# Performance work log

Measured on AMD Instinct MI355X. Metric: run time of the kernel, lower is better.

The kernel has to match this reference:

```python
import math
import jax, jax.numpy as jnp
import numpy as np

B, H, HKV, L, S, D = 1, 32, 8, 2048, 2048, 128
N_REP = H // HKV          # 4
SCALE = 1.0 / math.sqrt(D)


def setup_inputs() -> dict:
    key = jax.random.key(0)
    k1, k2, k3, k4 = jax.random.split(key, 4)
    query = jax.random.normal(k1, (B, H, L, D), dtype=jnp.float32)
    k_ = jax.random.normal(k2, (B, HKV, S, D), dtype=jnp.float32)
    v_ = jax.random.normal(k3, (B, HKV, S, D), dtype=jnp.float32)
    attn_mask = jax.random.normal(k4, (B, 1, L, S), dtype=jnp.float32)
    return {"query": query, "key": k_, "value": v_, "attn_mask": attn_mask}


def reference(query, key, value, attn_mask):
    # repeat_kv: Q -> [B, HKV, n_rep, L, D]; K/V stay [B, HKV, S, D]
    # (the torch code reshapes K/V to [B, HKV, 1, S, D]; broadcasting via
    # einsum is equivalent), mask unsqueezed at dim 1 -> [B, 1, 1, L, S].
    q = query.reshape(B, HKV, N_REP, L, D)
    scores = jnp.einsum("bkrld,bksd->bkrls", q, key)          # [B,HKV,n_rep,L,S]
    scores = scores + attn_mask[:, None]                        # broadcast add
    # softmax_fp8(x, dim=-1, invAttnHead=1/sqrt(D)) scales input by invAttnHead
    w = jax.nn.softmax(scores * SCALE, axis=-1)
    # dropout_p = 0.0 -> identity
    out = jnp.einsum("bkrls,bksd->bkrld", w, value)             # [B,HKV,n_rep,L,D]
    return out
```

## Files before the change

### kernel.cpp

```cpp
#include <hip/hip_runtime.h>

#define NH   32
#define NKV  8
#define LQ   2048
#define SK   2048
#define DH   128
#define BM   128
#define BN   64
#define KSTRIDE 136
#define VSTRIDE 72

typedef __attribute__((ext_vector_type(8)))  short bf8;
typedef __attribute__((ext_vector_type(4)))  float f4;
typedef __attribute__((ext_vector_type(16))) float f16v;

#if __has_builtin(__builtin_amdgcn_exp2f)
#define EXP2F(x) __builtin_amdgcn_exp2f(x)
#else
#define EXP2F(x) exp2f(x)
#endif

__device__ __forceinline__ unsigned int f2bf(float f) {
    unsigned int u = __builtin_bit_cast(unsigned int, f);
    u = (u + 0x7FFFu + ((u >> 16) & 1u)) >> 16;
    return u;
}

__global__ __launch_bounds__(256) void convert_k_kernel(
    const float* __restrict__ K, unsigned short* __restrict__ Kb)
{
    size_t base = ((size_t)blockIdx.x * 256 + threadIdx.x) * 8;
    float4 a = *(const float4*)(K + base);
    float4 b = *(const float4*)(K + base + 4);
    bf8 o;
    o[0] = (short)f2bf(a.x); o[1] = (short)f2bf(a.y);
    o[2] = (short)f2bf(a.z); o[3] = (short)f2bf(a.w);
    o[4] = (short)f2bf(b.x); o[5] = (short)f2bf(b.y);
    o[6] = (short)f2bf(b.z); o[7] = (short)f2bf(b.w);
    *(bf8*)(Kb + base) = o;
}

__global__ __launch_bounds__(256) void transpose_v_kernel(
    const float* __restrict__ V, unsigned short* __restrict__ VTb)
{
    __shared__ __align__(16) unsigned short Vl[DH * VSTRIDE];
    const int tid = threadIdx.x;
    const int kv  = blockIdx.x >> 5;
    const int s0  = (blockIdx.x & 31) * 64;
    const float* Vh = V + (size_t)kv * SK * DH;

    #pragma unroll
    for (int i = 0; i < 8; ++i) {
        int idx = tid * 4 + i * 1024;
        int s = idx >> 7, d = idx & 127;
        const float4 v4 = *(const float4*)(Vh + (size_t)(s0 + s) * DH + d);
        Vl[(d + 0) * VSTRIDE + s] = (unsigned short)f2bf(v4.x);
        Vl[(d + 1) * VSTRIDE + s] = (unsigned short)f2bf(v4.y);
        Vl[(d + 2) * VSTRIDE + s] = (unsigned short)f2bf(v4.z);
        Vl[(d + 3) * VSTRIDE + s] = (unsigned short)f2bf(v4.w);
    }
    __syncthreads();
    unsigned short* out = VTb + (size_t)kv * DH * SK;
    #pragma unroll
    for (int i = 0; i < 4; ++i) {
        int c = tid + i * 256;
        int d = c >> 3, s8 = (c & 7) * 8;
        *(bf8*)(out + (size_t)d * SK + s0 + s8) = *(const bf8*)(Vl + d * VSTRIDE + s8);
    }
}

__global__ __launch_bounds__(256, 2) void fattn_kernel(
    const float* __restrict__ Q, const unsigned short* __restrict__ Kb,
    const unsigned short* __restrict__ VTb, const float* __restrict__ M,
    float* __restrict__ O)
{
    __shared__ __align__(16) unsigned short Klds[2][BN * KSTRIDE];
    __shared__ __align__(16) unsigned short Vlds[2][DH * VSTRIDE];

    const int tid  = threadIdx.x;
    const int wave = tid >> 6;
    const int lane = tid & 63;
    const int l32  = lane & 31;
    const int hh   = lane >> 5;

    const int bx = blockIdx.x;
    const int h  = bx >> 4;
    const int lt = bx & 15;
    const int q0 = lt * BM;
    const int kv = h >> 2;

    const float*          Qh  = Q   + (size_t)h  * LQ * DH;
    const unsigned short* Kh  = Kb  + (size_t)kv * SK * DH;
    const unsigned short* VTh = VTb + (size_t)kv * DH * SK;

    const int sK0 = tid >> 4,        dK0 = (tid & 15) * 8;
    const int dV0 = tid >> 3,        sV0 = (tid & 7) * 8;

    const int qrow = q0 + wave * 32 + l32;
    const float* Mq = M + (size_t)qrow * SK;

    bf8 bQ[8];
    #pragma unroll
    for (int ks = 0; ks < 8; ++ks) {
        const float* qp = Qh + (size_t)qrow * DH + ks * 16 + hh * 8;
        float4 a = *(const float4*)(qp);
        float4 b = *(const float4*)(qp + 4);
        bQ[ks][0] = (short)f2bf(a.x); bQ[ks][1] = (short)f2bf(a.y);
        bQ[ks][2] = (short)f2bf(a.z); bQ[ks][3] = (short)f2bf(a.w);
        bQ[ks][4] = (short)f2bf(b.x); bQ[ks][5] = (short)f2bf(b.y);
        bQ[ks][6] = (short)f2bf(b.z); bQ[ks][7] = (short)f2bf(b.w);
    }

    f16v accO[4];
    #pragma unroll
    for (int nt = 0; nt < 4; ++nt)
        #pragma unroll
        for (int r = 0; r < 16; ++r) accO[nt][r] = 0.f;
    float lpart = 0.f;

    const float scale_log2e = 0.08838834764831845f * 1.4426950408889634f;

    bf8 kf[4], vf[4];
    #pragma unroll
    for (int c = 0; c < 4; ++c) {
        kf[c] = *(const bf8*)(Kh + (size_t)(sK0 + c * 16) * DH + dK0);
        vf[c] = *(const bf8*)(VTh + (size_t)(dV0 + c * 32) * SK + sV0);
    }
    #pragma unroll
    for (int c = 0; c < 4; ++c) {
        *(bf8*)(&Klds[0][(sK0 + c * 16) * KSTRIDE + dK0]) = kf[c];
        *(bf8*)(&Vlds[0][(dV0 + c * 32) * VSTRIDE + sV0]) = vf[c];
    }
    #pragma unroll
    for (int c = 0; c < 4; ++c) {
        kf[c] = *(const bf8*)(Kh + (size_t)(BN + sK0 + c * 16) * DH + dK0);
        vf[c] = *(const bf8*)(VTh + (size_t)(dV0 + c * 32) * SK + BN + sV0);
    }

    int buf = 0;
    for (int s0i = 0; s0i < SK; s0i += BN, buf ^= 1) {
        __syncthreads();

        float4 mv[2][4];
        #pragma unroll
        for (int mt = 0; mt < 2; ++mt)
            #pragma unroll
            for (int grp = 0; grp < 4; ++grp)
                mv[mt][grp] = *(const float4*)(Mq + s0i + mt * 32 + grp * 8 + hh * 4);

        const unsigned short* Kc = Klds[buf];
        const unsigned short* Vc = Vlds[buf];
        f16v accS[2];
        #pragma unroll
        for (int mt = 0; mt < 2; ++mt) {
            f16v a;
            #pragma unroll
            for (int r = 0; r < 16; ++r) a[r] = 0.f;
            #pragma unroll
            for (int ks = 0; ks < 8; ++ks) {
                bf8 aK = *(const bf8*)(Kc + (mt * 32 + l32) * KSTRIDE + ks * 16 + hh * 8);
                a = __builtin_amdgcn_mfma_f32_32x32x16_bf16(aK, bQ[ks], a, 0, 0, 0);
            }
            accS[mt] = a;
        }

        if (s0i + BN < SK) {
            #pragma unroll
            for (int c = 0; c < 4; ++c) {
                *(bf8*)(&Klds[buf ^ 1][(sK0 + c * 16) * KSTRIDE + dK0]) = kf[c];
                *(bf8*)(&Vlds[buf ^ 1][(dV0 + c * 32) * VSTRIDE + sV0]) = vf[c];
            }
            if (s0i + 2 * BN < SK) {
                #pragma unroll
                for (int c = 0; c < 4; ++c) {
                    kf[c] = *(const bf8*)(Kh + (size_t)(s0i + 2 * BN + sK0 + c * 16) * DH + dK0);
                    vf[c] = *(const bf8*)(VTh + (size_t)(dV0 + c * 32) * SK + s0i + 2 * BN + sV0);
                }
            }
        }

        unsigned int W[2][4][2];
        #pragma unroll
        for (int mt = 0; mt < 2; ++mt) {
            #pragma unroll
            for (int g = 0; g < 4; ++g) {
                float e0 = EXP2F((accS[mt][g * 4 + 0] + mv[mt][g].x) * scale_log2e);
                float e1 = EXP2F((accS[mt][g * 4 + 1] + mv[mt][g].y) * scale_log2e);
                float e2 = EXP2F((accS[mt][g * 4 + 2] + mv[mt][g].z) * scale_log2e);
                float e3 = EXP2F((accS[mt][g * 4 + 3] + mv[mt][g].w) * scale_log2e);
                lpart += (e0 + e1) + (e2 + e3);
                W[mt][g][0] = f2bf(e0) | (f2bf(e1) << 16);
                W[mt][g][1] = f2bf(e2) | (f2bf(e3) << 16);
            }
        }
        unsigned int R[2][4][2];
        #pragma unroll
        for (int mt = 0; mt < 2; ++mt)
            #pragma unroll
            for (int g = 0; g < 4; ++g)
                #pragma unroll
                for (int b = 0; b < 2; ++b)
                    R[mt][g][b] = (unsigned int)__shfl_xor((int)W[mt][g][b], 32);

        bf8 bP[4];
        #pragma unroll
        for (int ks = 0; ks < 4; ++ks) {
            const int mt = ks >> 1, b = (ks & 1) * 2;
            unsigned int lo0 = hh ? R[mt][b + 1][0] : W[mt][b][0];
            unsigned int lo1 = hh ? R[mt][b + 1][1] : W[mt][b][1];
            unsigned int hi0 = hh ? W[mt][b + 1][0] : R[mt][b][0];
            unsigned int hi1 = hh ? W[mt][b + 1][1] : R[mt][b][1];
            uint4 u = {lo0, lo1, hi0, hi1};
            bP[ks] = __builtin_bit_cast(bf8, u);
        }

        #pragma unroll
        for (int nt = 0; nt < 4; ++nt) {
            f16v a = accO[nt];
            #pragma unroll
            for (int ks = 0; ks < 4; ++ks) {
                bf8 aV = *(const bf8*)(Vc + (nt * 32 + l32) * VSTRIDE + ks * 16 + hh * 8);
                a = __builtin_amdgcn_mfma_f32_32x32x16_bf16(aV, bP[ks], a, 0, 0, 0);
            }
            accO[nt] = a;
        }
    }

    float l = lpart + __shfl_xor(lpart, 32);
    float inv = 1.0f / l;
    float* Op = O + (size_t)h * LQ * DH + (size_t)qrow * DH;
    #pragma unroll
    for (int nt = 0; nt < 4; ++nt) {
        #pragma unroll
        for (int grp = 0; grp < 4; ++grp) {
            int d = nt * 32 + grp * 8 + hh * 4;
            float4 o;
            o.x = accO[nt][grp * 4 + 0] * inv;
            o.y = accO[nt][grp * 4 + 1] * inv;
            o.z = accO[nt][grp * 4 + 2] * inv;
            o.w = accO[nt][grp * 4 + 3] * inv;
            *(float4*)(Op + d) = o;
        }
    }
}

extern "C" void kernel_launch(void* const* d_in, const int* in_sizes, int n_in,
                              void* d_out, int out_size, void* d_ws, size_t ws_size,
                              hipStream_t stream) {
    const float* Q = (const float*)d_in[0];
    const float* K = (const float*)d_in[1];
    const float* V = (const float*)d_in[2];
    const float* M = (const float*)d_in[3];
    float* O = (float*)d_out;

    unsigned short* Kb  = (unsigned short*)d_ws;
    unsigned short* VTb = Kb + (size_t)NKV * SK * DH;

    convert_k_kernel<<<dim3((NKV * SK * DH) / (256 * 8)), 256, 0, stream>>>(K, Kb);
    transpose_v_kernel<<<dim3(NKV * (SK / 64)), 256, 0, stream>>>(V, VTb);

    dim3 grid(NH * (LQ / BM));
    fattn_kernel<<<grid, 256, 0, stream>>>(Q, Kb, VTb, M, O);
}
```

Measured before the change: 202.5 us.

## Process two query tiles per wave to reuse K/V LDS fragments

Doubles the query block to 256 rows so each wave handles 64 query rows as two 32-row MFMA tiles sharing each K and V fragment loaded from LDS. This halves LDS reads per MFMA and amortizes mask/softmax overhead, at the cost of doubled accumulator registers and occupancy reduced to one block per CU. It also switches probability packing to a hardware packed bf16 conversion when available.

Result: slower. 256.8 us (+26.8%).

```diff
diff --git a/kernel.cpp b/kernel.cpp
--- a/kernel.cpp
+++ b/kernel.cpp
@@ -5,7 +5,7 @@
 #define LQ   2048
 #define SK   2048
 #define DH   128
-#define BM   128
+#define BM   256
 #define BN   64
 #define KSTRIDE 136
 #define VSTRIDE 72
@@ -24,6 +24,15 @@
     unsigned int u = __builtin_bit_cast(unsigned int, f);
     u = (u + 0x7FFFu + ((u >> 16) & 1u)) >> 16;
     return u;
+}
+
+__device__ __forceinline__ unsigned int packbf(float a, float b) {
+#if __has_builtin(__builtin_amdgcn_cvt_pk_bf16_f32)
+    auto r = __builtin_amdgcn_cvt_pk_bf16_f32(a, b);
+    unsigned int u; __builtin_memcpy(&u, &r, 4); return u;
+#else
+    return f2bf(a) | (f2bf(b) << 16);
+#endif
 }
 
 __global__ __launch_bounds__(256) void convert_k_kernel(
@@ -69,7 +78,7 @@
     }
 }
 
-__global__ __launch_bounds__(256, 2) void fattn_kernel(
+__global__ __launch_bounds__(256, 1) void fattn_kernel(
     const float* __restrict__ Q, const unsigned short* __restrict__ Kb,
     const unsigned short* __restrict__ VTb, const float* __restrict__ M,
     float* __restrict__ O)
@@ -84,8 +93,8 @@
     const int hh   = lane >> 5;
 
     const int bx = blockIdx.x;
-    const int h  = bx >> 4;
-    const int lt = bx & 15;
+    const int h  = bx >> 3;
+    const int lt = bx & 7;
     const int q0 = lt * BM;
     const int kv = h >> 2;
 
@@ -96,27 +105,35 @@
     const int sK0 = tid >> 4,        dK0 = (tid & 15) * 8;
     const int dV0 = tid >> 3,        sV0 = (tid & 7) * 8;
 
-    const int qrow = q0 + wave * 32 + l32;
-    const float* Mq = M + (size_t)qrow * SK;
-
-    bf8 bQ[8];
-    #pragma unroll
-    for (int ks = 0; ks < 8; ++ks) {
-        const float* qp = Qh + (size_t)qrow * DH + ks * 16 + hh * 8;
-        float4 a = *(const float4*)(qp);
-        float4 b = *(const float4*)(qp + 4);
-        bQ[ks][0] = (short)f2bf(a.x); bQ[ks][1] = (short)f2bf(a.y);
-        bQ[ks][2] = (short)f2bf(a.z); bQ[ks][3] = (short)f2bf(a.w);
-        bQ[ks][4] = (short)f2bf(b.x); bQ[ks][5] = (short)f2bf(b.y);
-        bQ[ks][6] = (short)f2bf(b.z); bQ[ks][7] = (short)f2bf(b.w);
-    }
-
-    f16v accO[4];
-    #pragma unroll
-    for (int nt = 0; nt < 4; ++nt)
-        #pragma unroll
-        for (int r = 0; r < 16; ++r) accO[nt][r] = 0.f;
-    float lpart = 0.f;
+    const int qrow0 = q0 + wave * 64 + l32;
+    const int qrow1 = qrow0 + 32;
+    const float* Mq0 = M + (size_t)qrow0 * SK;
+    const float* Mq1 = M + (size_t)qrow1 * SK;
+
+    bf8 bQ[2][8];
+    #pragma unroll
+    for (int qs = 0; qs < 2; ++qs) {
+        const float* Qr = Qh + (size_t)(qs ? qrow1 : qrow0) * DH;
+        #pragma unroll
+        for (int ks = 0; ks < 8; ++ks) {
+            const float* qp = Qr + ks * 16 + hh * 8;
+            float4 a = *(const float4*)(qp);
+            float4 b = *(const float4*)(qp + 4);
+            bQ[qs][ks][0] = (short)f2bf(a.x); bQ[qs][ks][1] = (short)f2bf(a.y);
+            bQ[qs][ks][2] = (short)f2bf(a.z); bQ[qs][ks][3] = (short)f2bf(a.w);
+            bQ[qs][ks][4] = (short)f2bf(b.x); bQ[qs][ks][5] = (short)f2bf(b.y);
+            bQ[qs][ks][6] = (short)f2bf(b.z); bQ[qs][ks][7] = (short)f2bf(b.w);
+        }
+    }
+
+    f16v accO[2][4];
+    #pragma unroll
+    for (int qs = 0; qs < 2; ++qs)
+        #pragma unroll
+        for (int nt = 0; nt < 4; ++nt)
+            #pragma unroll
+            for (int r = 0; r < 16; ++r) accO[qs][nt][r] = 0.f;
+    float lpart[2] = {0.f, 0.f};
 
     const float scale_log2e = 0.08838834764831845f * 1.4426950408889634f;
 
@@ -141,27 +158,32 @@
     for (int s0i = 0; s0i < SK; s0i += BN, buf ^= 1) {
         __syncthreads();
 
-        float4 mv[2][4];
+        float4 mv[2][2][4];
         #pragma unroll
         for (int mt = 0; mt < 2; ++mt)
             #pragma unroll
-            for (int grp = 0; grp < 4; ++grp)
-                mv[mt][grp] = *(const float4*)(Mq + s0i + mt * 32 + grp * 8 + hh * 4);
+            for (int grp = 0; grp < 4; ++grp) {
+                mv[0][mt][grp] = *(const float4*)(Mq0 + s0i + mt * 32 + grp * 8 + hh * 4);
+                mv[1][mt][grp] = *(const float4*)(Mq1 + s0i + mt * 32 + grp * 8 + hh * 4);
+            }
 
         const unsigned short* Kc = Klds[buf];
         const unsigned short* Vc = Vlds[buf];
-        f16v accS[2];
+        f16v accS[2][2];
+        #pragma unroll
+        for (int qs = 0; qs < 2; ++qs)
+            #pragma unroll
+            for (int mt = 0; mt < 2; ++mt)
+                #pragma unroll
+                for (int r = 0; r < 16; ++r) accS[qs][mt][r] = 0.f;
         #pragma unroll
         for (int mt = 0; mt < 2; ++mt) {
-            f16v a;
-            #pragma unroll
-            for (int r = 0; r < 16; ++r) a[r] = 0.f;
             #pragma unroll
             for (int ks = 0; ks < 8; ++ks) {
                 bf8 aK = *(const bf8*)(Kc + (mt * 32 + l32) * KSTRIDE + ks * 16 + hh * 8);
-                a = __builtin_amdgcn_mfma_f32_32x32x16_bf16(aK, bQ[ks], a, 0, 0, 0);
-            }
-            accS[mt] = a;
+                accS[0][mt] = __builtin_amdgcn_mfma_f32_32x32x16_bf16(aK, bQ[0][ks], accS[0][mt], 0, 0, 0);
+                accS[1][mt] = __builtin_amdgcn_mfma_f32_32x32x16_bf16(aK, bQ[1][ks], accS[1][mt], 0, 0, 0);
+            }
         }
 
         if (s0i + BN < SK) {
@@ -179,67 +201,71 @@
             }
         }
 
-        unsigned int W[2][4][2];
-        #pragma unroll
-        for (int mt = 0; mt < 2; ++mt) {
-            #pragma unroll
-            for (int g = 0; g < 4; ++g) {
-                float e0 = EXP2F((accS[mt][g * 4 + 0] + mv[mt][g].x) * scale_log2e);
-                float e1 = EXP2F((accS[mt][g * 4 + 1] + mv[mt][g].y) * scale_log2e);
-                float e2 = EXP2F((accS[mt][g * 4 + 2] + mv[mt][g].z) * scale_log2e);
-                float e3 = EXP2F((accS[mt][g * 4 + 3] + mv[mt][g].w) * scale_log2e);
-                lpart += (e0 + e1) + (e2 + e3);
-                W[mt][g][0] = f2bf(e0) | (f2bf(e1) << 16);
-                W[mt][g][1] = f2bf(e2) | (f2bf(e3) << 16);
-            }
-        }
-        unsigned int R[2][4][2];
-        #pragma unroll
-        for (int mt = 0; mt < 2; ++mt)
-            #pragma unroll
-            for (int g = 0; g < 4; ++g)
-                #pragma unroll
-                for (int b = 0; b < 2; ++b)
-                    R[mt][g][b] = (unsigned int)__shfl_xor((int)W[mt][g][b], 32);
-
-        bf8 bP[4];
-        #pragma unroll
-        for (int ks = 0; ks < 4; ++ks) {
-            const int mt = ks >> 1, b = (ks & 1) * 2;
-            unsigned int lo0 = hh ? R[mt][b + 1][0] : W[mt][b][0];
-            unsigned int lo1 = hh ? R[mt][b + 1][1] : W[mt][b][1];
-            unsigned int hi0 = hh ? W[mt][b + 1][0] : R[mt][b][0];
-            unsigned int hi1 = hh ? W[mt][b + 1][1] : R[mt][b][1];
-            uint4 u = {lo0, lo1, hi0, hi1};
-            bP[ks] = __builtin_bit_cast(bf8, u);
+        bf8 bP[2][4];
+        #pragma unroll
+        for (int qs = 0; qs < 2; ++qs) {
+            unsigned int W[2][4][2];
+            #pragma unroll
+            for (int mt = 0; mt < 2; ++mt) {
+                #pragma unroll
+                for (int g = 0; g < 4; ++g) {
+                    float e0 = EXP2F((accS[qs][mt][g * 4 + 0] + mv[qs][mt][g].x) * scale_log2e);
+                    float e1 = EXP2F((accS[qs][mt][g * 4 + 1] + mv[qs][mt][g].y) * scale_log2e);
+                    float e2 = EXP2F((accS[qs][mt][g * 4 + 2] + mv[qs][mt][g].z) * scale_log2e);
+                    float e3 = EXP2F((accS[qs][mt][g * 4 + 3] + mv[qs][mt][g].w) * scale_log2e);
+                    lpart[qs] += (e0 + e1) + (e2 + e3);
+                    W[mt][g][0] = packbf(e0, e1);
+                    W[mt][g][1] = packbf(e2, e3);
+                }
+            }
+            unsigned int R[2][4][2];
+            #pragma unroll
+            for (int mt = 0; mt < 2; ++mt)
+                #pragma unroll
+                for (int g = 0; g < 4; ++g)
+                    #pragma unroll
+                    for (int b = 0; b < 2; ++b)
+                        R[mt][g][b] = (unsigned int)__shfl_xor((int)W[mt][g][b], 32);
+            #pragma unroll
+            for (int ks = 0; ks < 4; ++ks) {
+                const int mt = ks >> 1, b = (ks & 1) * 2;
+                unsigned int lo0 = hh ? R[mt][b + 1][0] : W[mt][b][0];
+                unsigned int lo1 = hh ? R[mt][b + 1][1] : W[mt][b][1];
+                unsigned int hi0 = hh ? W[mt][b + 1][0] : R[mt][b][0];
+                unsigned int hi1 = hh ? W[mt][b + 1][1] : R[mt][b][1];
+                uint4 u = {lo0, lo1, hi0, hi1};
+                bP[qs][ks] = __builtin_bit_cast(bf8, u);
+            }
         }
 
         #pragma unroll
         for (int nt = 0; nt < 4; ++nt) {
-            f16v a = accO[nt];
             #pragma unroll
             for (int ks = 0; ks < 4; ++ks) {
                 bf8 aV = *(const bf8*)(Vc + (nt * 32 + l32) * VSTRIDE + ks * 16 + hh * 8);
-                a = __builtin_amdgcn_mfma_f32_32x32x16_bf16(aV, bP[ks], a, 0, 0, 0);
-            }
-            accO[nt] = a;
-        }
-    }
-
-    float l = lpart + __shfl_xor(lpart, 32);
-    float inv = 1.0f / l;
-    float* Op = O + (size_t)h * LQ * DH + (size_t)qrow * DH;
-    #pragma unroll
-    for (int nt = 0; nt < 4; ++nt) {
-        #pragma unroll
-        for (int grp = 0; grp < 4; ++grp) {
-            int d = nt * 32 + grp * 8 + hh * 4;
-            float4 o;
-            o.x = accO[nt][grp * 4 + 0] * inv;
-            o.y = accO[nt][grp * 4 + 1] * inv;
-            o.z = accO[nt][grp * 4 + 2] * inv;
-            o.w = accO[nt][grp * 4 + 3] * inv;
-            *(float4*)(Op + d) = o;
+                accO[0][nt] = __builtin_amdgcn_mfma_f32_32x32x16_bf16(aV, bP[0][ks], accO[0][nt], 0, 0, 0);
+                accO[1][nt] = __builtin_amdgcn_mfma_f32_32x32x16_bf16(aV, bP[1][ks], accO[1][nt], 0, 0, 0);
+            }
+        }
+    }
+
+    #pragma unroll
+    for (int qs = 0; qs < 2; ++qs) {
+        float l = lpart[qs] + __shfl_xor(lpart[qs], 32);
+        float inv = 1.0f / l;
+        float* Op = O + (size_t)h * LQ * DH + (size_t)(qs ? qrow1 : qrow0) * DH;
+        #pragma unroll
+        for (int nt = 0; nt < 4; ++nt) {
+            #pragma unroll
+            for (int grp = 0; grp < 4; ++grp) {
+                int d = nt * 32 + grp * 8 + hh * 4;
+                float4 o;
+                o.x = accO[qs][nt][grp * 4 + 0] * inv;
+                o.y = accO[qs][nt][grp * 4 + 1] * inv;
+                o.z = accO[qs][nt][grp * 4 + 2] * inv;
+                o.w = accO[qs][nt][grp * 4 + 3] * inv;
+                *(float4*)(Op + d) = o;
+            }
         }
     }
 }
```
